# Optimization experiments

Measured on AMD Instinct MI355X. Metric: run time of the kernel, lower is better.

## Reference

```python
import jax, jax.numpy as jnp
import numpy as np

N_IMG = 1024
N_VIEWS = 90


def _bilinear(img, yi, xi):
    """Bilinear sample img at float coords (yi=row, xi=col); 0 outside (skimage warp cval=0)."""
    n = img.shape[0]
    y0 = jnp.floor(yi)
    x0 = jnp.floor(xi)
    wy = yi - y0
    wx = xi - x0
    y0i = y0.astype(jnp.int32)
    x0i = x0.astype(jnp.int32)

    def get(yy, xx):
        valid = (yy >= 0) & (yy < n) & (xx >= 0) & (xx < n)
        v = img[jnp.clip(yy, 0, n - 1), jnp.clip(xx, 0, n - 1)]
        return jnp.where(valid, v, jnp.zeros((), img.dtype))

    v00 = get(y0i, x0i)
    v01 = get(y0i, x0i + 1)
    v10 = get(y0i + 1, x0i)
    v11 = get(y0i + 1, x0i + 1)
    return (v00 * (1 - wy) * (1 - wx) + v01 * (1 - wy) * wx
            + v10 * wy * (1 - wx) + v11 * wy * wx)


def radon_jax(image, theta_deg):
    """skimage.transform.radon(image, theta, circle=True) equivalent.
    Rotate image by each angle (bilinear, about center = N//2, inverse map as in
    skimage warp) and sum over rows. Returns sinogram [N, n_angles]."""
    n = image.shape[0]
    center = n // 2
    ang = jnp.deg2rad(theta_deg.astype(image.dtype))
    cos_a = jnp.cos(ang)  # [A]
    sin_a = jnp.sin(ang)
    coords = jnp.arange(n, dtype=image.dtype)
    X, Y = jnp.meshgrid(coords, coords)  # X = col (x), Y = row (y), [N, N]

    def rotate_and_sum(ca, sa):
        # inverse map: src = R @ dst (homogeneous, (x, y) order) as in skimage radon
        x_in = ca * X + sa * Y - center * (ca + sa - 1)
        y_in = -sa * X + ca * Y - center * (ca - sa - 1)
        rotated = _bilinear(image, y_in, x_in)  # [N, N]
        return rotated.sum(axis=0)  # sum over rows -> projection [N]

    sino = jax.vmap(rotate_and_sum)(cos_a, sin_a)  # [A, N]
    return sino.T  # [N, A] to match skimage radon layout


def setup_inputs() -> dict:
    key = jax.random.key(0)
    k1, _ = jax.random.split(key)
    x = jax.random.normal(k1, (N_IMG, N_IMG), dtype=jnp.float32)
    theta = jnp.arange(N_VIEWS, dtype=jnp.float32) * 2.0  # 0..178 deg, 2-deg spacing
    return {"x": x, "theta": theta}


def reference(x, theta):
    return radon_jax(x, theta)
```

## Files before the change

kernel.cpp:

```cpp
#include <hip/hip_runtime.h>

#define N_IMG   1024
#define N_VIEWS 90
#define CENTER  512
#define TILE    64
#define NYB     (N_IMG / TILE)
#define NTHREADS 512
#define NWAVES   8
#define YPT      (TILE / NWAVES)
#define TILE_WORDS 9216

__device__ __forceinline__ void map_coords(float ca, float sa, float cx, float cy,
                                           float Xf, float Yf,
                                           float& x_in, float& y_in) {
    const float fx0 = fmaf(ca, Xf, cx);
    const float fy0 = fmaf(-sa, Xf, cy);
    x_in = fmaf(sa, Yf, fx0);
    y_in = fmaf(ca, Yf, fy0);
}

__device__ __forceinline__ void gload_lds4(const float* g, float* l) {
    __builtin_amdgcn_global_load_lds((const __attribute__((address_space(1))) void*)g,
                                     (__attribute__((address_space(3))) void*)l, 4, 0, 0);
}
__device__ __forceinline__ void gload_lds16(const float* g, float* l) {
    __builtin_amdgcn_global_load_lds((const __attribute__((address_space(1))) void*)g,
                                     (__attribute__((address_space(3))) void*)l, 16, 0, 0);
}

template<int STRIDE>
__device__ __forceinline__ float sample_tile(const float* __restrict__ tile,
                                             float sa, float ca,
                                             float x_in, float y_in, float basef) {
    float acc = 0.0f;
    const float Sf = (float)STRIDE;
    #pragma unroll
    for (int i = 0; i < YPT; ++i) {
        const float x0f = floorf(x_in);
        const float y0f = floorf(y_in);
        const float wx  = x_in - x0f;
        const float wy  = y_in - y0f;
        const int li = (int)(fmaf(y0f, Sf, x0f) + basef);
        const float t00 = tile[li];
        const float t01 = tile[li + 1];
        const float t10 = tile[li + STRIDE];
        const float t11 = tile[li + STRIDE + 1];
        const float top = fmaf(wx, t01 - t00, t00);
        const float bot = fmaf(wx, t11 - t10, t10);
        acc += fmaf(wy, bot - top, top);
        x_in += sa; y_in += ca;
    }
    return acc;
}

__global__ __launch_bounds__(NTHREADS) void radon_tile(const float* __restrict__ img,
                                                       const float* __restrict__ theta,
                                                       float* __restrict__ partial,
                                                       float* __restrict__ out,
                                                       int mode) {
    __shared__ float tile[TILE_WORDS];
    __shared__ float fpar[4];
    __shared__ int   ipar[8];

    const int a  = blockIdx.z;
    const int X0 = blockIdx.x * TILE;
    const int Y0 = blockIdx.y * TILE;
    const int tid  = threadIdx.x;
    const int lane = tid & 63;
    const int wv   = tid >> 6;

    if (wv == 0) {
        const float ang = theta[a] * 0.017453292519943295f;
        float sa, ca;
        __sincosf(ang, &sa, &ca);
        const float cx = (float)CENTER * (1.0f - ca - sa);
        const float cy = (float)CENTER * (1.0f - ca + sa);

        float x00, y00, x01, y01, x10, y10, x11, y11;
        map_coords(ca, sa, cx, cy, (float)X0,        (float)Y0,        x00, y00);
        map_coords(ca, sa, cx, cy, (float)(X0 + 63), (float)Y0,        x01, y01);
        map_coords(ca, sa, cx, cy, (float)X0,        (float)(Y0 + 63), x10, y10);
        map_coords(ca, sa, cx, cy, (float)(X0 + 63), (float)(Y0 + 63), x11, y11);
        const float xmin = fminf(fminf(x00, x01), fminf(x10, x11));
        const float xmax = fmaxf(fmaxf(x00, x01), fmaxf(x10, x11));
        const float ymin = fminf(fminf(y00, y01), fminf(y10, y11));
        const float ymax = fmaxf(fmaxf(y00, y01), fmaxf(y10, y11));

        const int ix0_raw = (int)floorf(xmin);
        const int ix1_raw = (int)floorf(xmax) + 1;
        const int iy0_raw = (int)floorf(ymin);
        const int iy1_raw = (int)floorf(ymax) + 1;

        const bool empty = (ix1_raw < 0) || (ix0_raw > N_IMG - 1) ||
                           (iy1_raw < 0) || (iy0_raw > N_IMG - 1);
        const bool interior = (ix0_raw >= 0) && (ix1_raw <= N_IMG - 1) &&
                              (iy0_raw >= 0) && (iy1_raw <= N_IMG - 1);

        int path = (fabsf(ca) > 0.7072f) ? 0 : ((ca > 0.0f) ? 1 : 2);
        int iy0w, win, dB = 0, ry0 = 0, nrows = 0;
        if (interior) {
            iy0w = iy0_raw;
            if (path == 0) {
                win = min(ix0_raw & ~3, N_IMG - 96);
            } else {
                win = min(ix0_raw, N_IMG - 64);
                dB  = max(win, ix1_raw - 63) - win;
            }
            nrows = iy1_raw - iy0_raw + 1;
        } else {
            iy0w = iy0_raw;
            win  = ix0_raw & ~3;
            ry0  = max(0, iy0_raw);
            nrows = min(N_IMG - 1, iy1_raw) - ry0 + 1;
        }
        if (tid == 0) {
            fpar[0] = sa; fpar[1] = ca; fpar[2] = cx; fpar[3] = cy;
            ipar[0] = iy0w; ipar[1] = nrows; ipar[2] = win; ipar[3] = dB;
            ipar[4] = path;
            ipar[5] = empty ? 1 : (interior ? 2 : 0);
            ipar[6] = ry0;
        }
    }
    __syncthreads();

    float* __restrict__ pslot = partial + ((size_t)(a * NYB + blockIdx.y) << 10) + X0;
    const int flags = ipar[5];

    if (flags & 1) {
        if (mode == 0 && tid < 64) pslot[tid] = 0.0f;
        return;
    }

    const float sa = fpar[0], ca = fpar[1], cx = fpar[2], cy = fpar[3];
    const int iy0 = ipar[0], nrows = ipar[1], win = ipar[2], dB = ipar[3];
    const int path = ipar[4];
    const int S = (path == 0) ? 96 : ((path == 1) ? 95 : 97);

    if (flags & 2) {
        if (path == 0) {
            const int D = nrows * 96;
            for (int o = wv * 256; o < D; o += NWAVES * 256) {
                const int d = o + 4 * lane;
                const int r = (unsigned)d / 96u;
                const int c = d - r * 96;
                const int gr = min(iy0 + r, N_IMG - 1);
                gload_lds16(img + (size_t)gr * N_IMG + win + c, tile + o);
            }
        } else {
            const float* g = img + (size_t)(iy0 + wv) * N_IMG + win + lane;
            float* l = tile + wv * S;
            for (int r = wv; r < nrows; r += NWAVES) {
                gload_lds4(g, l);
                if (dB > 0) gload_lds4(g + dB, l + dB);
                g += NWAVES * N_IMG;
                l += NWAVES * S;
            }
        }
    } else {
        for (int o4 = tid; o4 < TILE_WORDS / 4; o4 += NTHREADS)
            *(float4*)(tile + 4 * o4) = make_float4(0.f, 0.f, 0.f, 0.f);
        __syncthreads();
        const int ry0 = ipar[6];
        const int cx0 = max(0, win);
        const int cxe = min(N_IMG - 1, win + 94);
        const int wIn = cxe - cx0 + 1;
        const int n4  = wIn >> 2;
        const int items = nrows * 24;
        for (int idx = tid; idx < items; idx += NTHREADS) {
            const int r  = (unsigned)idx / 24u;
            const int c4 = idx - r * 24;
            const int gy = ry0 + r;
            float* dst = tile + (gy - iy0) * S + (cx0 - win) + 4 * c4;
            const float* src = img + (size_t)gy * N_IMG + cx0 + 4 * c4;
            if (c4 < n4) {
                *(float4*)dst = *(const float4*)src;
            } else if (c4 == n4) {
                for (int j = 0; j < (wIn & 3); ++j) dst[j] = src[j];
            }
        }
    }
    __syncthreads();

    const float Xf  = (float)(X0 + lane);
    const float fx0 = fmaf(ca, Xf, cx);
    const float fy0 = fmaf(-sa, Xf, cy);
    const float Ybf = (float)(Y0 + wv * YPT);
    const float x_in = fmaf(sa, Ybf, fx0);
    const float y_in = fmaf(ca, Ybf, fy0);
    const float basef = -(float)(iy0 * S + win);

    float acc;
    if (path == 0)      acc = sample_tile<96>(tile, sa, ca, x_in, y_in, basef);
    else if (path == 1) acc = sample_tile<95>(tile, sa, ca, x_in, y_in, basef);
    else                acc = sample_tile<97>(tile, sa, ca, x_in, y_in, basef);

    __syncthreads();
    tile[wv * 64 + lane] = acc;
    __syncthreads();
    if (wv == 0) {
        float s = 0.0f;
        #pragma unroll
        for (int w = 0; w < NWAVES; ++w) s += tile[w * 64 + lane];
        if (mode == 0) pslot[lane] = s;
        else           atomicAdd(&out[(X0 + lane) * N_VIEWS + a], s);
    }
}

__global__ __launch_bounds__(256) void reduce_partials(const float* __restrict__ partial,
                                                       float* __restrict__ out) {
    const int g = blockIdx.x * 256 + threadIdx.x;
    const int a = g >> 10;
    const int X = g & 1023;
    float s = 0.0f;
    #pragma unroll
    for (int yb = 0; yb < NYB; ++yb)
        s += partial[((size_t)(a * NYB + yb) << 10) + X];
    out[X * N_VIEWS + a] = s;
}

extern "C" void kernel_launch(void* const* d_in, const int* in_sizes, int n_in,
                              void* d_out, int out_size, void* d_ws, size_t ws_size,
                              hipStream_t stream) {
    const float* img   = (const float*)d_in[0];
    const float* theta = (const float*)d_in[1];
    float* out     = (float*)d_out;
    float* partial = (float*)d_ws;

    const size_t needed = (size_t)N_VIEWS * NYB * N_IMG * sizeof(float);
    const int mode = (ws_size >= needed) ? 0 : 1;
    if (mode == 1)
        hipMemsetAsync(d_out, 0, (size_t)out_size * sizeof(float), stream);

    dim3 grid(N_IMG / TILE, N_IMG / TILE, N_VIEWS);
    radon_tile<<<grid, NTHREADS, 0, stream>>>(img, theta, partial, out, mode);

    if (mode == 0)
        reduce_partials<<<(N_VIEWS * N_IMG) / 256, 256, 0, stream>>>(partial, out);
}
```

Baseline: 141.2 us.

## Pick per-angle LDS row stride to avoid bank conflicts and batch tile loads

Chooses the LDS row stride per angle (96 or 104 for the wide path, 97 or 99 for the negative-cosine path) using a heuristic that measures how close the per-step address delta lands to a multiple of 32 banks. The goal is to cut LDS bank conflicts during bilinear gathers. The sampling loop is restructured to compute four indices first and then issue all sixteen LDS loads together, which exposes more memory-level parallelism. It also enlarges the tile buffer and adds a launch-bounds occupancy hint, at the cost of more template instantiations and code size, and some risk of higher register pressure or lower occupancy from the larger LDS use.

```diff
diff --git a/kernel.cpp b/kernel.cpp
--- a/kernel.cpp
+++ b/kernel.cpp
@@ -8,7 +8,7 @@
 #define NTHREADS 512
 #define NWAVES   8
 #define YPT      (TILE / NWAVES)
-#define TILE_WORDS 9216
+#define TILE_WORDS 9856
 
 __device__ __forceinline__ void map_coords(float ca, float sa, float cx, float cy,
                                            float Xf, float Yf,
@@ -28,6 +28,11 @@
                                      (__attribute__((address_space(3))) void*)l, 16, 0, 0);
 }
 
+__device__ __forceinline__ float stride_bad(float sa, float ca, float S) {
+    const float t = (ca - sa * S) * 0.03125f;
+    return fabsf(t - rintf(t));
+}
+
 template<int STRIDE>
 __device__ __forceinline__ float sample_tile(const float* __restrict__ tile,
                                              float sa, float ca,
@@ -35,29 +40,54 @@
     float acc = 0.0f;
     const float Sf = (float)STRIDE;
     #pragma unroll
-    for (int i = 0; i < YPT; ++i) {
-        const float x0f = floorf(x_in);
-        const float y0f = floorf(y_in);
-        const float wx  = x_in - x0f;
-        const float wy  = y_in - y0f;
-        const int li = (int)(fmaf(y0f, Sf, x0f) + basef);
-        const float t00 = tile[li];
-        const float t01 = tile[li + 1];
-        const float t10 = tile[li + STRIDE];
-        const float t11 = tile[li + STRIDE + 1];
-        const float top = fmaf(wx, t01 - t00, t00);
-        const float bot = fmaf(wx, t11 - t10, t10);
-        acc += fmaf(wy, bot - top, top);
-        x_in += sa; y_in += ca;
+    for (int half = 0; half < 2; ++half) {
+        int   li[4];
+        float wx[4], wy[4];
+        #pragma unroll
+        for (int j = 0; j < 4; ++j) {
+            const float x0f = floorf(x_in);
+            const float y0f = floorf(y_in);
+            wx[j] = x_in - x0f;
+            wy[j] = y_in - y0f;
+            li[j] = (int)(fmaf(y0f, Sf, x0f) + basef);
+            x_in += sa; y_in += ca;
+        }
+        float t00[4], t01[4], t10[4], t11[4];
+        #pragma unroll
+        for (int j = 0; j < 4; ++j) {
+            t00[j] = tile[li[j]];
+            t01[j] = tile[li[j] + 1];
+            t10[j] = tile[li[j] + STRIDE];
+            t11[j] = tile[li[j] + STRIDE + 1];
+        }
+        #pragma unroll
+        for (int j = 0; j < 4; ++j) {
+            const float top = fmaf(wx[j], t01[j] - t00[j], t00[j]);
+            const float bot = fmaf(wx[j], t11[j] - t10[j], t10[j]);
+            acc += fmaf(wy[j], bot - top, top);
+        }
     }
     return acc;
 }
 
-__global__ __launch_bounds__(NTHREADS) void radon_tile(const float* __restrict__ img,
-                                                       const float* __restrict__ theta,
-                                                       float* __restrict__ partial,
-                                                       float* __restrict__ out,
-                                                       int mode) {
+template<int STRIDE>
+__device__ __forceinline__ void stage_wide(const float* __restrict__ img, float* buf,
+                                           int lane, int wv, int iy0, int nrows, int win) {
+    const int D = nrows * STRIDE;
+    for (int o = wv * 256; o < D; o += NWAVES * 256) {
+        const int d = o + 4 * lane;
+        const int r = (unsigned)d / (unsigned)STRIDE;
+        const int c = d - r * STRIDE;
+        const int gr = min(iy0 + r, N_IMG - 1);
+        gload_lds16(img + (size_t)gr * N_IMG + win + c, buf + o);
+    }
+}
+
+__global__ __launch_bounds__(NTHREADS, 8) void radon_tile(const float* __restrict__ img,
+                                                          const float* __restrict__ theta,
+                                                          float* __restrict__ partial,
+                                                          float* __restrict__ out,
+                                                          int mode) {
     __shared__ float tile[TILE_WORDS];
     __shared__ float fpar[4];
     __shared__ int   ipar[8];
@@ -96,12 +126,18 @@
         const bool interior = (ix0_raw >= 0) && (ix1_raw <= N_IMG - 1) &&
                               (iy0_raw >= 0) && (iy1_raw <= N_IMG - 1);
 
-        int path = (fabsf(ca) > 0.7072f) ? 0 : ((ca > 0.0f) ? 1 : 2);
+        const bool wide = (fabsf(ca) > 0.7072f);
+        int S;
+        if (wide)            S = (stride_bad(sa, ca, 104.f) > stride_bad(sa, ca, 96.f)) ? 104 : 96;
+        else if (ca > 0.0f)  S = 95;
+        else                 S = (stride_bad(sa, ca, 99.f) > stride_bad(sa, ca, 97.f)) ? 99 : 97;
+
+        int ix0 = max(0, ix0_raw), ix1 = min(N_IMG - 1, ix1_raw);
         int iy0w, win, dB = 0, ry0 = 0, nrows = 0;
         if (interior) {
             iy0w = iy0_raw;
-            if (path == 0) {
-                win = min(ix0_raw & ~3, N_IMG - 96);
+            if (wide) {
+                win = min(ix0_raw & ~3, N_IMG - S);
             } else {
                 win = min(ix0_raw, N_IMG - 64);
                 dB  = max(win, ix1_raw - 63) - win;
@@ -116,10 +152,11 @@
         if (tid == 0) {
             fpar[0] = sa; fpar[1] = ca; fpar[2] = cx; fpar[3] = cy;
             ipar[0] = iy0w; ipar[1] = nrows; ipar[2] = win; ipar[3] = dB;
-            ipar[4] = path;
+            ipar[4] = S;
             ipar[5] = empty ? 1 : (interior ? 2 : 0);
             ipar[6] = ry0;
         }
+        (void)ix0; (void)ix1;
     }
     __syncthreads();
 
@@ -133,19 +170,13 @@
 
     const float sa = fpar[0], ca = fpar[1], cx = fpar[2], cy = fpar[3];
     const int iy0 = ipar[0], nrows = ipar[1], win = ipar[2], dB = ipar[3];
-    const int path = ipar[4];
-    const int S = (path == 0) ? 96 : ((path == 1) ? 95 : 97);
+    const int S = ipar[4];
 
     if (flags & 2) {
-        if (path == 0) {
-            const int D = nrows * 96;
-            for (int o = wv * 256; o < D; o += NWAVES * 256) {
-                const int d = o + 4 * lane;
-                const int r = (unsigned)d / 96u;
-                const int c = d - r * 96;
-                const int gr = min(iy0 + r, N_IMG - 1);
-                gload_lds16(img + (size_t)gr * N_IMG + win + c, tile + o);
-            }
+        if (S == 96) {
+            stage_wide<96>(img, tile, lane, wv, iy0, nrows, win);
+        } else if (S == 104) {
+            stage_wide<104>(img, tile, lane, wv, iy0, nrows, win);
         } else {
             const float* g = img + (size_t)(iy0 + wv) * N_IMG + win + lane;
             float* l = tile + wv * S;
@@ -190,9 +221,11 @@
     const float basef = -(float)(iy0 * S + win);
 
     float acc;
-    if (path == 0)      acc = sample_tile<96>(tile, sa, ca, x_in, y_in, basef);
-    else if (path == 1) acc = sample_tile<95>(tile, sa, ca, x_in, y_in, basef);
-    else                acc = sample_tile<97>(tile, sa, ca, x_in, y_in, basef);
+    if (S == 96)       acc = sample_tile<96>(tile, sa, ca, x_in, y_in, basef);
+    else if (S == 95)  acc = sample_tile<95>(tile, sa, ca, x_in, y_in, basef);
+    else if (S == 97)  acc = sample_tile<97>(tile, sa, ca, x_in, y_in, basef);
+    else if (S == 99)  acc = sample_tile<99>(tile, sa, ca, x_in, y_in, basef);
+    else               acc = sample_tile<104>(tile, sa, ca, x_in, y_in, basef);
 
     __syncthreads();
     tile[wv * 64 + lane] = acc;
```

Result: slower. 148.0 us (+4.8%).
